# Optimization experiments

Measured on AMD Instinct MI355X. Metric: run time of the kernel, lower is better.

The kernel has to match this reference:

```python
import jax, jax.numpy as jnp
import numpy as np

B, S, D, H = 2, 2048, 1024, 16
MAX_DIST = 1024


def setup_inputs() -> dict:
    key = jax.random.key(0)
    ks = jax.random.split(key, 7)
    w = lambda k, shape: jax.random.normal(k, shape, jnp.float32) * 0.02
    return {
        "x": jax.random.normal(ks[0], (B, S, D), jnp.float32),
        "Wq": w(ks[1], (D, D)), "bq": jnp.zeros((D,), jnp.float32),
        "Wk": w(ks[2], (D, D)),
        "Wv": w(ks[3], (D, D)), "bv": jnp.zeros((D,), jnp.float32),
        "Wo": w(ks[4], (D, D)), "bo": jnp.zeros((D,), jnp.float32),
        "pos_bias": w(ks[5], (2 * MAX_DIST - 1, H)),
        "max_dist": MAX_DIST,
    }


def reference(x, Wq, bq, Wk, Wv, bv, Wo, bo, pos_bias, max_dist):
    b, s, d_model = x.shape
    h = pos_bias.shape[1]
    hd = d_model // h  # head dim
    scale = hd ** -0.25  # module's scale applied to (QK^T + rel_bias)

    split = lambda t: t.reshape(b, s, h, hd).transpose(0, 2, 1, 3)  # [b,h,s,hd]
    q = split(x @ Wq + bq)
    k = split(x @ Wk)          # key has no bias
    v = split(x @ Wv + bv)

    # raw QK^T (unscaled), as in the module
    scores = jnp.einsum('bhqd,bhkd->bhqk', q, k)

    # relative-position bias gather: clamp(i-j) -> table index
    pos = jnp.arange(s)[:, None] - jnp.arange(s)[None, :]
    pos = jnp.clip(pos, -max_dist + 1, max_dist - 1) + max_dist - 1
    rel_bias = pos_bias[pos].transpose(2, 0, 1)[None]  # [1,h,s,s]

    # SDPA with attn_mask = (scores + rel_bias)*scale adds it on top of QK^T/sqrt(hd)
    logits = scores * (1.0 / jnp.sqrt(jnp.float32(hd))) + (scores + rel_bias) * scale
    w = jax.nn.softmax(logits, axis=-1)

    out = jnp.einsum('bhqk,bhkd->bhqd', w, v)
    out = out.transpose(0, 2, 1, 3).reshape(b, s, d_model)
    return out @ Wo + bo
```

## Files before the change

kernel.cpp:

```cpp
#include <hip/hip_runtime.h>
#include <hip/hip_bf16.h>
#include <cstddef>
#include <cstdint>

#define BATCH   2
#define S_LEN   2048
#define D_MODEL 1024
#define NH      16
#define HD      64
#define MAXD    1024

#define SCORE_SCALE 0.47855339059327373f
#define BIAS_SCALE  0.35355339059327373f
#define FIXM 8.0f
#define LOG2E 1.4426950408889634f

typedef __attribute__((ext_vector_type(8))) short bf16x8;
typedef __attribute__((ext_vector_type(4))) short bf16x4;
typedef __attribute__((ext_vector_type(4))) float f32x4;

static __device__ __forceinline__ unsigned short f2bf(float f) {
    __hip_bfloat16 h = __float2bfloat16(f);
    return *reinterpret_cast<unsigned short*>(&h);
}

#define GLDS(gp, lp) __builtin_amdgcn_global_load_lds( \
    (const __attribute__((address_space(1))) void*)(gp), \
    (__attribute__((address_space(3))) void*)(lp), 16, 0, 0)

__global__ __launch_bounds__(256) void prep(
    const float* __restrict__ x,
    const float* __restrict__ Wq, const float* __restrict__ Wk,
    const float* __restrict__ Wv, const float* __restrict__ Wo,
    const float* __restrict__ pos_bias,
    unsigned short* __restrict__ xb, unsigned short* __restrict__ Wqkvt,
    unsigned short* __restrict__ Wot,
    float* __restrict__ pb_t)
{
    __shared__ float t[32][33];
    const int bx = blockIdx.x, tid = threadIdx.x;

    if (bx < 2048) {
        const size_t i = ((size_t)bx * 256 + tid) * 8;
        const float4 a = *(const float4*)(x + i);
        const float4 b = *(const float4*)(x + i + 4);
        unsigned short u[8] = {f2bf(a.x), f2bf(a.y), f2bf(a.z), f2bf(a.w),
                               f2bf(b.x), f2bf(b.y), f2bf(b.z), f2bf(b.w)};
        *(uint4*)(xb + i) = *(const uint4*)u;
    } else if (bx < 6144) {
        const int bx2 = bx - 2048;
        const int z = bx2 >> 10, inner = bx2 & 1023;
        const int gx = inner & 31, gy = inner >> 5;
        const float* W = (z == 0) ? Wq : (z == 1) ? Wk : (z == 2) ? Wv : Wo;
        unsigned short* hi = (z < 3) ? Wqkvt + (size_t)z * 1024 * 1024 : Wot;
        const int bxx = gx * 32, byy = gy * 32;
        const int tx = tid & 31, ty = tid >> 5;
        #pragma unroll
        for (int i = 0; i < 4; i++)
            t[ty + 8 * i][tx] = W[(size_t)(byy + ty + 8 * i) * 1024 + bxx + tx];
        __syncthreads();
        #pragma unroll
        for (int i = 0; i < 4; i++) {
            const float v = t[tx][ty + 8 * i];
            const size_t o = (size_t)(bxx + ty + 8 * i) * 1024 + byy + tx;
            hi[o] = f2bf(v);
        }
    } else {
        const int o0 = (bx - 6144) * 1024 + tid * 4;
        float v[4];
        #pragma unroll
        for (int j = 0; j < 4; j++) {
            const int o = o0 + j;
            const int hh = o >> 12, ii = o & 4095;
            int rel = ii - 2047;
            rel = min(max(rel, -(MAXD - 1)), MAXD - 1);
            v[j] = (BIAS_SCALE * pos_bias[(size_t)(rel + MAXD - 1) * NH + hh] - FIXM) * LOG2E;
        }
        *(float4*)&pb_t[o0] = *(const float4*)v;
    }
}

#define GBM 128
#define GBN 128
#define GBK 32

__global__ __launch_bounds__(256) void gemm_qkv(
    const unsigned short* __restrict__ A, const unsigned short* __restrict__ Bt,
    const float* __restrict__ bq, const float* __restrict__ bv,
    unsigned short* __restrict__ Cout)
{
    const int K = 1024;
    __shared__ __align__(16) unsigned short As[GBM][GBK];
    __shared__ __align__(16) unsigned short Bs[GBN][GBK];

    const int tid = threadIdx.x;
    const int wave = tid >> 6, lane = tid & 63;
    const int quad = lane >> 4, cl = lane & 15;
    const int wm = (wave & 1) * 64, wn = (wave >> 1) * 64;
    const int bm = blockIdx.y * GBM, bn = blockIdx.x * GBN;

    const int sr = wave * 32 + (lane >> 2);
    const int sc = (lane & 3) * 8;
    const unsigned short* aS0 = A  + (size_t)(bm + sr) * K + sc;
    const unsigned short* aS1 = aS0 + (size_t)16 * K;
    const unsigned short* bS0 = Bt + (size_t)(bn + sr) * K + sc;
    const unsigned short* bS1 = bS0 + (size_t)16 * K;
    unsigned short* aD0 = &As[wave * 32][0];
    unsigned short* aD1 = &As[wave * 32 + 16][0];
    unsigned short* bD0 = &Bs[wave * 32][0];
    unsigned short* bD1 = &Bs[wave * 32 + 16][0];

    f32x4 acc[4][4];
    #pragma unroll
    for (int mi = 0; mi < 4; mi++)
        #pragma unroll
        for (int ni = 0; ni < 4; ni++)
            #pragma unroll
            for (int r = 0; r < 4; r++) acc[mi][ni][r] = 0.f;

    for (int k0 = 0; k0 < K; k0 += GBK) {
        __syncthreads();
        GLDS(aS0, aD0); GLDS(aS1, aD1);
        GLDS(bS0, bD0); GLDS(bS1, bD1);
        aS0 += GBK; aS1 += GBK; bS0 += GBK; bS1 += GBK;
        __syncthreads();

        bf16x8 af[4], bf[4];
        #pragma unroll
        for (int mi = 0; mi < 4; mi++)
            af[mi] = *(const bf16x8*)&As[wm + mi * 16 + cl][quad * 8];
        #pragma unroll
        for (int ni = 0; ni < 4; ni++)
            bf[ni] = *(const bf16x8*)&Bs[wn + ni * 16 + cl][quad * 8];
        #pragma unroll
        for (int mi = 0; mi < 4; mi++)
            #pragma unroll
            for (int ni = 0; ni < 4; ni++)
                acc[mi][ni] = __builtin_amdgcn_mfma_f32_16x16x32_bf16(
                    af[mi], bf[ni], acc[mi][ni], 0, 0, 0);
    }

    #pragma unroll
    for (int ni = 0; ni < 4; ni++) {
        const int coln = bn + wn + ni * 16 + cl;
        const int region = coln >> 10, c = coln & 1023;
        const float bs = (region == 0) ? bq[c] : (region == 2) ? bv[c] : 0.f;
        #pragma unroll
        for (int mi = 0; mi < 4; mi++) {
            const int row0 = bm + wm + mi * 16 + quad * 4;
            if (region == 2) {
                const int hh = c >> 6, d = c & 63;
                const int bb = row0 >> 11, s0 = row0 & 2047;
                unsigned short u[4];
                #pragma unroll
                for (int r = 0; r < 4; r++) u[r] = f2bf(acc[mi][ni][r] + bs);
                unsigned short* dst = Cout + (size_t)8 * 1024 * 1024
                    + (((size_t)bb * NH + hh) * HD + d) * S_LEN + s0;
                *(uint2*)dst = *(const uint2*)u;
            } else {
                unsigned short* dst = Cout + (size_t)region * 4 * 1024 * 1024;
                #pragma unroll
                for (int r = 0; r < 4; r++)
                    dst[(size_t)(row0 + r) * 1024 + c] = f2bf(acc[mi][ni][r] + bs);
            }
        }
    }
}

#define TQB 128
#define TKB 64

__global__ __launch_bounds__(256) void attn_mfma(
    const unsigned short* __restrict__ Q, const unsigned short* __restrict__ K,
    const unsigned short* __restrict__ VT, const float* __restrict__ pb_t,
    unsigned short* __restrict__ O)
{
    const int qt = blockIdx.x, h = blockIdx.y, b = blockIdx.z;
    const int tid  = threadIdx.x;
    const int wave = tid >> 6, lane = tid & 63;
    const int quad = lane >> 4, col = lane & 15;
    const int qbase = qt * TQB;
    const int qw = qbase + wave * 32;

    __shared__ __align__(16) unsigned short Ks[2][TKB][HD];
    __shared__ __align__(16) unsigned short Vs[2][HD][TKB];

    bf16x8 qf[2][2];
    #pragma unroll
    for (int f = 0; f < 2; f++) {
        const unsigned short* qp =
            &Q[((size_t)(b * S_LEN) + qw + f * 16 + col) * D_MODEL + h * HD + quad * 8];
        qf[f][0] = *(const bf16x8*)qp;
        qf[f][1] = *(const bf16x8*)(qp + 32);
    }

    f32x4 accO[2][4];
    #pragma unroll
    for (int f = 0; f < 2; f++)
        #pragma unroll
        for (int nb = 0; nb < 4; nb++)
            #pragma unroll
            for (int r = 0; r < 4; r++) accO[f][nb][r] = 0.f;
    f32x4 accL[2];
    #pragma unroll
    for (int f = 0; f < 2; f++)
        #pragma unroll
        for (int r = 0; r < 4; r++) accL[f][r] = 0.f;
    const bf16x4 vone = {(short)16256, (short)16256, (short)16256, (short)16256};

    const int s0 = tid, s1 = 256 + tid;
    const int kr0 = s0 >> 3, kj0 = (s0 & 7) ^ (kr0 & 7);
    const int kr1 = s1 >> 3, kj1 = (s1 & 7) ^ (kr1 & 7);
    const unsigned short* kS0 = K + ((size_t)(b * S_LEN) + kr0) * D_MODEL + h * HD + kj0 * 8;
    const unsigned short* kS1 = K + ((size_t)(b * S_LEN) + kr1) * D_MODEL + h * HD + kj1 * 8;
    const size_t vbase = ((size_t)(b * NH + h) * HD) * S_LEN;
    const unsigned short* vS0 = VT + vbase + (size_t)kr0 * S_LEN + kj0 * 8;
    const unsigned short* vS1 = VT + vbase + (size_t)kr1 * S_LEN + kj1 * 8;
    unsigned short* kD = &Ks[0][0][0] + wave * 512;
    unsigned short* vD = &Vs[0][0][0] + wave * 512;

    const float* pbh = pb_t + h * 4096;
    const float* pb_lane = pbh + (qw + col - quad * 4 + 2047);
    const float SC2 = SCORE_SCALE * LOG2E;
    const int jsw = col & 7;

    GLDS(kS0, kD); GLDS(kS1, kD + 2048);
    GLDS(vS0, vD); GLDS(vS1, vD + 2048);
    kS0 += (size_t)TKB * D_MODEL; kS1 += (size_t)TKB * D_MODEL;
    vS0 += TKB; vS1 += TKB;

    float biasA[2][16], biasB[2][16];
    #pragma unroll
    for (int f = 0; f < 2; f++)
        #pragma unroll
        for (int nb = 0; nb < 4; nb++)
            #pragma unroll
            for (int r = 0; r < 4; r++)
                biasA[f][nb * 4 + r] = pb_lane[f * 16 - (nb * 16 + r)];
    pb_lane -= TKB;

    __syncthreads();

    const int NT = S_LEN / TKB;

#define ATT_TILE(T, P, BC, BN)                                                \
  {                                                                           \
    if ((T) != NT - 1) {                                                      \
      GLDS(kS0, kD + ((P) ^ 1) * 4096); GLDS(kS1, kD + ((P) ^ 1) * 4096 + 2048); \
      GLDS(vS0, vD + ((P) ^ 1) * 4096); GLDS(vS1, vD + ((P) ^ 1) * 4096 + 2048); \
      kS0 += (size_t)TKB * D_MODEL; kS1 += (size_t)TKB * D_MODEL;             \
      vS0 += TKB; vS1 += TKB;                                                 \
      _Pragma("unroll")                                                       \
      for (int f = 0; f < 2; f++)                                             \
        _Pragma("unroll")                                                     \
        for (int nb = 0; nb < 4; nb++)                                        \
          _Pragma("unroll")                                                   \
          for (int r = 0; r < 4; r++)                                         \
            BN[f][nb * 4 + r] = pb_lane[f * 16 - (nb * 16 + r)];              \
      pb_lane -= TKB;                                                         \
    }                                                                         \
    f32x4 accS[2][4];                                                         \
    _Pragma("unroll")                                                         \
    for (int f = 0; f < 2; f++)                                               \
      _Pragma("unroll")                                                       \
      for (int nb = 0; nb < 4; nb++)                                          \
        _Pragma("unroll")                                                     \
        for (int r = 0; r < 4; r++) accS[f][nb][r] = 0.f;                     \
    _Pragma("unroll")                                                         \
    for (int kk = 0; kk < 2; kk++)                                            \
      _Pragma("unroll")                                                       \
      for (int nb = 0; nb < 4; nb++) {                                        \
        const bf16x8 kf = *(const bf16x8*)                                    \
            &Ks[P][nb * 16 + col][((kk * 4 + quad) ^ jsw) * 8];               \
        accS[0][nb] = __builtin_amdgcn_mfma_f32_16x16x32_bf16(                \
            kf, qf[0][kk], accS[0][nb], 0, 0, 0);                             \
        accS[1][nb] = __builtin_amdgcn_mfma_f32_16x16x32_bf16(                \
            kf, qf[1][kk], accS[1][nb], 0, 0, 0);                             \
      }                                                                       \
    bf16x4 pf[2][4];                                                          \
    _Pragma("unroll")                                                         \
    for (int f = 0; f < 2; f++)                                               \
      _Pragma("unroll")                                                       \
      for (int nb = 0; nb < 4; nb++) {                                        \
        float pr[4];                                                          \
        _Pragma("unroll")                                                     \
        for (int r = 0; r < 4; r++)                                           \
          pr[r] = __builtin_amdgcn_exp2f(                                     \
              fmaf(accS[f][nb][r], SC2, BC[f][nb * 4 + r]));                  \
        const __hip_bfloat162 h0 = __float22bfloat162_rn(make_float2(pr[0], pr[1])); \
        const __hip_bfloat162 h1 = __float22bfloat162_rn(make_float2(pr[2], pr[3])); \
        uint2 w;                                                              \
        w.x = *(const unsigned int*)&h0;                                      \
        w.y = *(const unsigned int*)&h1;                                      \
        union { uint2 u; bf16x4 v; } cv;                                      \
        cv.u = w;                                                             \
        pf[f][nb] = cv.v;                                                     \
        accL[f] = __builtin_amdgcn_mfma_f32_16x16x16bf16_1k(                  \
            vone, pf[f][nb], accL[f], 0, 0, 0);                               \
      }                                                                       \
    _Pragma("unroll")                                                         \
    for (int s = 0; s < 4; s++)                                               \
      _Pragma("unroll")                                                       \
      for (int nb = 0; nb < 4; nb++) {                                        \
        const bf16x4 vf = *(const bf16x4*)                                    \
            &Vs[P][nb * 16 + col][(((2 * s + (quad >> 1)) ^ jsw) * 8) + (quad & 1) * 4]; \
        accO[0][nb] = __builtin_amdgcn_mfma_f32_16x16x16bf16_1k(              \
            vf, pf[0][s], accO[0][nb], 0, 0, 0);                              \
        accO[1][nb] = __builtin_amdgcn_mfma_f32_16x16x16bf16_1k(              \
            vf, pf[1][s], accO[1][nb], 0, 0, 0);                              \
      }                                                                       \
    __syncthreads();                                                          \
  }

    for (int t = 0; t < NT; t += 2) {
        ATT_TILE(t,     0, biasA, biasB);
        ATT_TILE(t + 1, 1, biasB, biasA);
    }
#undef ATT_TILE

    #pragma unroll
    for (int f = 0; f < 2; f++) {
        const float inv = 1.0f / accL[f][0];
        const size_t row = (size_t)(b * S_LEN) + qw + f * 16 + col;
        #pragma unroll
        for (int nb = 0; nb < 4; nb++) {
            unsigned short u[4];
            #pragma unroll
            for (int r = 0; r < 4; r++) u[r] = f2bf(accO[f][nb][r] * inv);
            *(uint2*)&O[row * D_MODEL + h * HD + nb * 16 + quad * 4] = *(const uint2*)u;
        }
    }
}

#define OBM 64
#define OBN 128

__global__ __launch_bounds__(256) void gemm_out(
    const unsigned short* __restrict__ A, const unsigned short* __restrict__ Bt,
    const float* __restrict__ bias, float* __restrict__ Cout)
{
    const int N = 1024, Kd = 1024;
    __shared__ __align__(16) unsigned short As[OBM][GBK];
    __shared__ __align__(16) unsigned short Bs[OBN][GBK];

    const int tid = threadIdx.x;
    const int wave = tid >> 6, lane = tid & 63;
    const int quad = lane >> 4, cl = lane & 15;
    const int wm = (wave & 1) * 32, wn = (wave >> 1) * 64;
    const int bm = blockIdx.y * OBM, bn = blockIdx.x * OBN;

    const int ar = tid >> 2, ac = (tid & 3) * 8;
    const unsigned short* aS = A + (size_t)(bm + ar) * Kd + ac;
    const unsigned short* hS0 = Bt + (size_t)(bn + ar) * Kd + ac;
    const unsigned short* hS1 = hS0 + (size_t)64 * Kd;
    unsigned short* aD  = &As[0][0] + wave * 512;
    unsigned short* hD0 = &Bs[0][0] + wave * 512;
    unsigned short* hD1 = hD0 + 2048;

    f32x4 acc[2][4];
    #pragma unroll
    for (int mi = 0; mi < 2; mi++)
        #pragma unroll
        for (int ni = 0; ni < 4; ni++)
            #pragma unroll
            for (int r = 0; r < 4; r++) acc[mi][ni][r] = 0.f;

    for (int k0 = 0; k0 < Kd; k0 += GBK) {
        __syncthreads();
        GLDS(aS, aD);
        GLDS(hS0, hD0); GLDS(hS1, hD1);
        aS += GBK; hS0 += GBK; hS1 += GBK;
        __syncthreads();

        bf16x8 af[2], bh[4];
        #pragma unroll
        for (int mi = 0; mi < 2; mi++)
            af[mi] = *(const bf16x8*)&As[wm + mi * 16 + cl][quad * 8];
        #pragma unroll
        for (int ni = 0; ni < 4; ni++)
            bh[ni] = *(const bf16x8*)&Bs[wn + ni * 16 + cl][quad * 8];
        #pragma unroll
        for (int mi = 0; mi < 2; mi++)
            #pragma unroll
            for (int ni = 0; ni < 4; ni++)
                acc[mi][ni] = __builtin_amdgcn_mfma_f32_16x16x32_bf16(
                    af[mi], bh[ni], acc[mi][ni], 0, 0, 0);
    }

    #pragma unroll
    for (int ni = 0; ni < 4; ni++) {
        const int coln = bn + wn + ni * 16 + cl;
        const float bs = bias[coln];
        #pragma unroll
        for (int mi = 0; mi < 2; mi++) {
            const int row0 = bm + wm + mi * 16 + quad * 4;
            #pragma unroll
            for (int r = 0; r < 4; r++)
                Cout[(size_t)(row0 + r) * N + coln] = acc[mi][ni][r] + bs;
        }
    }
}

extern "C" void kernel_launch(void* const* d_in, const int* in_sizes, int n_in,
                              void* d_out, int out_size, void* d_ws, size_t ws_size,
                              hipStream_t stream)
{
    const float* x        = (const float*)d_in[0];
    const float* Wq       = (const float*)d_in[1];
    const float* bq       = (const float*)d_in[2];
    const float* Wk       = (const float*)d_in[3];
    const float* Wv       = (const float*)d_in[4];
    const float* bv       = (const float*)d_in[5];
    const float* Wo       = (const float*)d_in[6];
    const float* bo       = (const float*)d_in[7];
    const float* pos_bias = (const float*)d_in[8];
    float* out = (float*)d_out;

    const size_t ELEMS  = (size_t)BATCH * S_LEN * D_MODEL;
    const size_t WELEMS = (size_t)D_MODEL * D_MODEL;
    unsigned short* xb     = (unsigned short*)d_ws;
    unsigned short* Wqkvt  = xb + ELEMS;
    unsigned short* Wot    = Wqkvt + 3 * WELEMS;
    unsigned short* QKV    = Wot + WELEMS;
    unsigned short* Qb     = QKV;
    unsigned short* Kb     = Qb + ELEMS;
    unsigned short* VTb    = Kb + ELEMS;
    unsigned short* Ab     = VTb + ELEMS;
    float* pb_t            = (float*)(Ab + ELEMS);

    prep<<<6208, 256, 0, stream>>>(x, Wq, Wk, Wv, Wo, pos_bias,
                                   xb, Wqkvt, Wot, pb_t);

    gemm_qkv<<<dim3(3072 / GBN, 4096 / GBM), 256, 0, stream>>>(
        xb, Wqkvt, bq, bv, QKV);

    attn_mfma<<<dim3(S_LEN / TQB, NH, BATCH), 256, 0, stream>>>(
        Qb, Kb, VTb, pb_t, Ab);

    gemm_out<<<dim3(1024 / OBN, 4096 / OBM), 256, 0, stream>>>(
        Ab, Wot, bo, out);
}
```

Baseline: 208.0 us.

## Split attention key range across two wave groups and merge partials in LDS

The attention kernel now launches 512 threads per block, and each group of 4 waves processes half of the key sequence (1024 keys) for the same 128 query rows. Each group writes its unnormalized output and row sums to shared memory, where they are added and then normalized. This doubles the waves working per block and halves the serial key loop, which should help latency hiding on a grid of only 512 blocks. In exchange, LDS use grows to 64KB per block, there is an extra merge step, and the bias prefetch double-buffering is dropped in favour of loads inside each tile. The merge by plain addition is valid because the softmax uses a fixed offset instead of a running max.

```diff
diff --git a/kernel.cpp b/kernel.cpp
--- a/kernel.cpp
+++ b/kernel.cpp
@@ -170,7 +170,7 @@
 #define TQB 128
 #define TKB 64
 
-__global__ __launch_bounds__(256) void attn_mfma(
+__global__ __launch_bounds__(512, 4) void attn_mfma(
     const unsigned short* __restrict__ Q, const unsigned short* __restrict__ K,
     const unsigned short* __restrict__ VT, const float* __restrict__ pb_t,
     unsigned short* __restrict__ O)
@@ -178,12 +178,13 @@
     const int qt = blockIdx.x, h = blockIdx.y, b = blockIdx.z;
     const int tid  = threadIdx.x;
     const int wave = tid >> 6, lane = tid & 63;
+    const int g = wave >> 2, w4 = wave & 3;
     const int quad = lane >> 4, col = lane & 15;
     const int qbase = qt * TQB;
-    const int qw = qbase + wave * 32;
-
-    __shared__ __align__(16) unsigned short Ks[2][TKB][HD];
-    __shared__ __align__(16) unsigned short Vs[2][HD][TKB];
+    const int qw = qbase + w4 * 32;
+
+    __shared__ __align__(16) unsigned char smem[65536];
+    unsigned char* const base_g = smem + g * 32768;
 
     bf16x8 qf[2][2];
     #pragma unroll
@@ -208,19 +209,22 @@
         for (int r = 0; r < 4; r++) accL[f][r] = 0.f;
     const bf16x4 vone = {(short)16256, (short)16256, (short)16256, (short)16256};
 
-    const int s0 = tid, s1 = 256 + tid;
+    const int tg = tid & 255;
+    const int s0 = tg, s1 = 256 + tg;
     const int kr0 = s0 >> 3, kj0 = (s0 & 7) ^ (kr0 & 7);
     const int kr1 = s1 >> 3, kj1 = (s1 & 7) ^ (kr1 & 7);
-    const unsigned short* kS0 = K + ((size_t)(b * S_LEN) + kr0) * D_MODEL + h * HD + kj0 * 8;
-    const unsigned short* kS1 = K + ((size_t)(b * S_LEN) + kr1) * D_MODEL + h * HD + kj1 * 8;
+    const unsigned short* kS0 =
+        K + ((size_t)(b * S_LEN) + g * 1024 + kr0) * D_MODEL + h * HD + kj0 * 8;
+    const unsigned short* kS1 =
+        K + ((size_t)(b * S_LEN) + g * 1024 + kr1) * D_MODEL + h * HD + kj1 * 8;
     const size_t vbase = ((size_t)(b * NH + h) * HD) * S_LEN;
-    const unsigned short* vS0 = VT + vbase + (size_t)kr0 * S_LEN + kj0 * 8;
-    const unsigned short* vS1 = VT + vbase + (size_t)kr1 * S_LEN + kj1 * 8;
-    unsigned short* kD = &Ks[0][0][0] + wave * 512;
-    unsigned short* vD = &Vs[0][0][0] + wave * 512;
+    const unsigned short* vS0 = VT + vbase + (size_t)kr0 * S_LEN + g * 1024 + kj0 * 8;
+    const unsigned short* vS1 = VT + vbase + (size_t)kr1 * S_LEN + g * 1024 + kj1 * 8;
+    unsigned short* kD = (unsigned short*)base_g + w4 * 512;
+    unsigned short* vD = (unsigned short*)(base_g + 8192) + w4 * 512;
 
     const float* pbh = pb_t + h * 4096;
-    const float* pb_lane = pbh + (qw + col - quad * 4 + 2047);
+    const float* pb_lane = pbh + (qw + col - quad * 4 - g * 1024 + 2047);
     const float SC2 = SCORE_SCALE * LOG2E;
     const int jsw = col & 7;
 
@@ -228,37 +232,29 @@
     GLDS(vS0, vD); GLDS(vS1, vD + 2048);
     kS0 += (size_t)TKB * D_MODEL; kS1 += (size_t)TKB * D_MODEL;
     vS0 += TKB; vS1 += TKB;
-
-    float biasA[2][16], biasB[2][16];
-    #pragma unroll
-    for (int f = 0; f < 2; f++)
-        #pragma unroll
-        for (int nb = 0; nb < 4; nb++)
-            #pragma unroll
-            for (int r = 0; r < 4; r++)
-                biasA[f][nb * 4 + r] = pb_lane[f * 16 - (nb * 16 + r)];
-    pb_lane -= TKB;
-
     __syncthreads();
 
-    const int NT = S_LEN / TKB;
-
-#define ATT_TILE(T, P, BC, BN)                                                \
+    const int NT = 1024 / TKB;
+
+#define ATT_TILE(T, P)                                                        \
   {                                                                           \
     if ((T) != NT - 1) {                                                      \
-      GLDS(kS0, kD + ((P) ^ 1) * 4096); GLDS(kS1, kD + ((P) ^ 1) * 4096 + 2048); \
-      GLDS(vS0, vD + ((P) ^ 1) * 4096); GLDS(vS1, vD + ((P) ^ 1) * 4096 + 2048); \
+      GLDS(kS0, kD + ((P) ^ 1) * 8192); GLDS(kS1, kD + ((P) ^ 1) * 8192 + 2048); \
+      GLDS(vS0, vD + ((P) ^ 1) * 8192); GLDS(vS1, vD + ((P) ^ 1) * 8192 + 2048); \
       kS0 += (size_t)TKB * D_MODEL; kS1 += (size_t)TKB * D_MODEL;             \
       vS0 += TKB; vS1 += TKB;                                                 \
+    }                                                                         \
+    float bias_c[2][16];                                                      \
+    _Pragma("unroll")                                                         \
+    for (int f = 0; f < 2; f++)                                               \
       _Pragma("unroll")                                                       \
-      for (int f = 0; f < 2; f++)                                             \
+      for (int nb = 0; nb < 4; nb++)                                          \
         _Pragma("unroll")                                                     \
-        for (int nb = 0; nb < 4; nb++)                                        \
-          _Pragma("unroll")                                                   \
-          for (int r = 0; r < 4; r++)                                         \
-            BN[f][nb * 4 + r] = pb_lane[f * 16 - (nb * 16 + r)];              \
-      pb_lane -= TKB;                                                         \
-    }                                                                         \
+        for (int r = 0; r < 4; r++)                                           \
+          bias_c[f][nb * 4 + r] = pb_lane[f * 16 - (nb * 16 + r)];            \
+    pb_lane -= TKB;                                                           \
+    const unsigned short* Kp = (const unsigned short*)(base_g + (P) * 16384); \
+    const unsigned short* Vp = (const unsigned short*)(base_g + (P) * 16384 + 8192); \
     f32x4 accS[2][4];                                                         \
     _Pragma("unroll")                                                         \
     for (int f = 0; f < 2; f++)                                               \
@@ -271,7 +267,7 @@
       _Pragma("unroll")                                                       \
       for (int nb = 0; nb < 4; nb++) {                                        \
         const bf16x8 kf = *(const bf16x8*)                                    \
-            &Ks[P][nb * 16 + col][((kk * 4 + quad) ^ jsw) * 8];               \
+            &Kp[(nb * 16 + col) * 64 + (((kk * 4 + quad) ^ jsw) * 8)];        \
         accS[0][nb] = __builtin_amdgcn_mfma_f32_16x16x32_bf16(                \
             kf, qf[0][kk], accS[0][nb], 0, 0, 0);                             \
         accS[1][nb] = __builtin_amdgcn_mfma_f32_16x16x32_bf16(                \
@@ -286,7 +282,7 @@
         _Pragma("unroll")                                                     \
         for (int r = 0; r < 4; r++)                                           \
           pr[r] = __builtin_amdgcn_exp2f(                                     \
-              fmaf(accS[f][nb][r], SC2, BC[f][nb * 4 + r]));                  \
+              fmaf(accS[f][nb][r], SC2, bias_c[f][nb * 4 + r]));              \
         const __hip_bfloat162 h0 = __float22bfloat162_rn(make_float2(pr[0], pr[1])); \
         const __hip_bfloat162 h1 = __float22bfloat162_rn(make_float2(pr[2], pr[3])); \
         uint2 w;                                                              \
@@ -303,7 +299,7 @@
       _Pragma("unroll")                                                       \
       for (int nb = 0; nb < 4; nb++) {                                        \
         const bf16x4 vf = *(const bf16x4*)                                    \
-            &Vs[P][nb * 16 + col][(((2 * s + (quad >> 1)) ^ jsw) * 8) + (quad & 1) * 4]; \
+            &Vp[(nb * 16 + col) * 64 + (((2 * s + (quad >> 1)) ^ jsw) * 8) + (quad & 1) * 4]; \
         accO[0][nb] = __builtin_amdgcn_mfma_f32_16x16x16bf16_1k(              \
             vf, pf[0][s], accO[0][nb], 0, 0, 0);                              \
         accO[1][nb] = __builtin_amdgcn_mfma_f32_16x16x16bf16_1k(              \
@@ -313,21 +309,38 @@
   }
 
     for (int t = 0; t < NT; t += 2) {
-        ATT_TILE(t,     0, biasA, biasB);
-        ATT_TILE(t + 1, 1, biasB, biasA);
+        ATT_TILE(t,     0);
+        ATT_TILE(t + 1, 1);
     }
 #undef ATT_TILE
 
-    #pragma unroll
-    for (int f = 0; f < 2; f++) {
-        const float inv = 1.0f / accL[f][0];
-        const size_t row = (size_t)(b * S_LEN) + qw + f * 16 + col;
-        #pragma unroll
-        for (int nb = 0; nb < 4; nb++) {
-            unsigned short u[4];
-            #pragma unroll
-            for (int r = 0; r < 4; r++) u[r] = f2bf(accO[f][nb][r] * inv);
-            *(uint2*)&O[row * D_MODEL + h * HD + nb * 16 + quad * 4] = *(const uint2*)u;
+    float* const Mo = (float*)smem;
+    const int idx = (w4 * 64 + lane) * 34;
+    if (g == 1) {
+        #pragma unroll
+        for (int f = 0; f < 2; f++) {
+            #pragma unroll
+            for (int nb = 0; nb < 4; nb++)
+                #pragma unroll
+                for (int r = 0; r < 4; r++)
+                    Mo[idx + f * 16 + nb * 4 + r] = accO[f][nb][r];
+            Mo[idx + 32 + f] = accL[f][0];
+        }
+    }
+    __syncthreads();
+    if (g == 0) {
+        #pragma unroll
+        for (int f = 0; f < 2; f++) {
+            const float inv = 1.0f / (accL[f][0] + Mo[idx + 32 + f]);
+            const size_t row = (size_t)(b * S_LEN) + qw + f * 16 + col;
+            #pragma unroll
+            for (int nb = 0; nb < 4; nb++) {
+                unsigned short u[4];
+                #pragma unroll
+                for (int r = 0; r < 4; r++)
+                    u[r] = f2bf((accO[f][nb][r] + Mo[idx + f * 16 + nb * 4 + r]) * inv);
+                *(uint2*)&O[row * D_MODEL + h * HD + nb * 16 + quad * 4] = *(const uint2*)u;
+            }
         }
     }
 }
@@ -434,7 +447,7 @@
     gemm_qkv<<<dim3(3072 / GBN, 4096 / GBM), 256, 0, stream>>>(
         xb, Wqkvt, bq, bv, QKV);
 
-    attn_mfma<<<dim3(S_LEN / TQB, NH, BATCH), 256, 0, stream>>>(
+    attn_mfma<<<dim3(S_LEN / TQB, NH, BATCH), 512, 0, stream>>>(
         Qb, Kb, VTb, pb_t, Ab);
 
     gemm_out<<<dim3(1024 / OBN, 4096 / OBM), 256, 0, stream>>>(
```

Measured after the change: 200.4 us. 1.04x faster.
